# Performance work log

Hardware: AMD Instinct MI355X
Metric: run time of the kernel (lower is better)

Reference implementation:

```python
import jax, jax.numpy as jnp
import numpy as np

T, B, IDIM, CDIM, N, M = 512, 64, 256, 512, 128, 64
EPS = 1e-8


def setup_inputs() -> dict:
    key = jax.random.key(0)
    ks = jax.random.split(key, 16)
    stdev = 5.0 / np.sqrt(IDIM + M + CDIM)
    u = lambda k, s: jax.random.uniform(k, s, jnp.float32, -stdev, stdev)
    return {
        'embs': jax.random.normal(ks[0], (T, B, IDIM), jnp.float32),
        'W_ih': u(ks[1], (4 * CDIM, IDIM + M)),
        'W_hh': u(ks[2], (4 * CDIM, CDIM)),
        'b_ih': jnp.zeros((4 * CDIM,), jnp.float32),
        'b_hh': jnp.zeros((4 * CDIM,), jnp.float32),
        'W_kr': jax.random.normal(ks[3], (M, CDIM), jnp.float32) * 0.05,
        'b_kr': jnp.zeros((M,), jnp.float32),
        'w_br': jax.random.normal(ks[4], (CDIM,), jnp.float32) * 0.05,
        'W_kw': jax.random.normal(ks[5], (M, CDIM), jnp.float32) * 0.05,
        'b_kw': jnp.zeros((M,), jnp.float32),
        'w_bw': jax.random.normal(ks[6], (CDIM,), jnp.float32) * 0.05,
        'W_e': jax.random.normal(ks[7], (M, CDIM), jnp.float32) * 0.05,
        'b_e': jnp.zeros((M,), jnp.float32),
        'W_a': jax.random.normal(ks[8], (M, IDIM), jnp.float32) * 0.05,
        'b_a': jnp.zeros((M,), jnp.float32),
        'h0': jax.random.normal(ks[9], (CDIM,), jnp.float32) * 0.05,
        'c0': jax.random.normal(ks[10], (CDIM,), jnp.float32) * 0.05,
        'r0': jax.random.normal(ks[11], (M,), jnp.float32) * 0.02,
        'mem0': jax.random.normal(ks[12], (N, M), jnp.float32) * 0.01,
    }


def _address(Mem, k, beta):
    # Mem: [B,N,M], k: [B,M], beta: [B] -> content weights [B,N]
    sim = jnp.einsum('bnm,bm->bn', Mem, k)
    denom = jnp.linalg.norm(Mem, axis=2) * jnp.linalg.norm(k, axis=1)[:, None] + EPS
    return jax.nn.softmax(beta[:, None] * (sim / denom), axis=1)


def reference(embs, W_ih, W_hh, b_ih, b_hh, W_kr, b_kr, w_br, W_kw, b_kw,
              w_bw, W_e, b_e, W_a, b_a, h0, c0, r0, mem0):
    bsz = embs.shape[1]
    h = jnp.broadcast_to(h0, (bsz, CDIM))
    c = jnp.broadcast_to(c0, (bsz, CDIM))
    r = jnp.broadcast_to(r0, (bsz, M))
    Mem = jnp.broadcast_to(mem0, (bsz, N, M))

    def step(carry, emb):
        h, c, r, Mem = carry
        x = jnp.concatenate([emb, r], axis=1)            # [B, idim+M]
        gates = x @ W_ih.T + b_ih + h @ W_hh.T + b_hh    # [B, 4*cdim]
        i, f, g, o = jnp.split(gates, 4, axis=1)          # torch LSTM gate order
        i, f, o = jax.nn.sigmoid(i), jax.nn.sigmoid(f), jax.nn.sigmoid(o)
        g = jnp.tanh(g)
        c = f * c + i * g
        h = o * jnp.tanh(c)
        co = h                                            # controller output
        # write (erase/add, NTM content addressing)
        kw = jnp.tanh(co @ W_kw.T + b_kw)
        ww = _address(Mem, kw, jax.nn.softplus(co @ w_bw))
        e = jax.nn.sigmoid(co @ W_e.T + b_e)
        a = jnp.tanh(emb @ W_a.T + b_a)
        Mem = Mem * (1.0 - ww[:, :, None] * e[:, None, :]) + ww[:, :, None] * a[:, None, :]
        # read
        kr = jnp.tanh(co @ W_kr.T + b_kr)
        wr = _address(Mem, kr, jax.nn.softplus(co @ w_br))
        r = jnp.einsum('bn,bnm->bm', wr, Mem)
        out = jnp.concatenate([co, r], axis=1)            # [B, cdim+M]
        return (h, c, r, Mem), out

    _, os = jax.lax.scan(step, (h, c, r, Mem), embs)
    return os  # [T, B, cdim+M]
```

## Files before the change

kernel.cpp:

```cpp
#include <hip/hip_runtime.h>

#define TT 512
#define BB 64
#define IDIM 256
#define CDIM 512
#define NMEM 128
#define MDIM 64
#define KTOT 832
#define ODIM 576
#define NROWS 2048
#define NA 256
#define NB 64

struct Params {
  const float* embs; const float* W_ih; const float* W_hh; const float* b_ih; const float* b_hh;
  const float* W_kr; const float* b_kr; const float* w_br; const float* W_kw; const float* b_kw;
  const float* w_bw; const float* W_e; const float* b_e; const float* W_a; const float* b_a;
  const float* h0; const float* c0; const float* r0; const float* mem0;
  float* out;
  unsigned* flags;
  float* Wopt;
  float* h_buf;
  float* r_buf;
};

__device__ __forceinline__ float sigmoidf_(float x) { return 1.0f / (1.0f + __expf(-x)); }
__device__ __forceinline__ float tanhf_(float x) {
  float e = __expf(-2.0f * fabsf(x));
  float t = (1.0f - e) / (1.0f + e);
  return copysignf(t, x);
}
__device__ __forceinline__ float softplusf_(float x) {
  return (x > 20.0f) ? x : log1pf(__expf(x));
}
__device__ __forceinline__ float wred_sum(float v) {
#pragma unroll
  for (int off = 32; off > 0; off >>= 1) v += __shfl_xor(v, off, 64);
  return v;
}
__device__ __forceinline__ float wred_max(float v) {
#pragma unroll
  for (int off = 32; off > 0; off >>= 1) v = fmaxf(v, __shfl_xor(v, off, 64));
  return v;
}
__device__ __forceinline__ unsigned wred_minu(unsigned v) {
#pragma unroll
  for (int off = 32; off > 0; off >>= 1) {
    unsigned o = (unsigned)__shfl_xor((int)v, off, 64);
    v = (o < v) ? o : v;
  }
  return v;
}

__device__ __forceinline__ unsigned flag_ld(const unsigned* f) {
  return __hip_atomic_load(f, __ATOMIC_RELAXED, __HIP_MEMORY_SCOPE_AGENT);
}
__device__ __forceinline__ void st_wt(float* p, float v) {
  __hip_atomic_store(p, v, __ATOMIC_RELAXED, __HIP_MEMORY_SCOPE_AGENT);
}
__device__ __forceinline__ void flag_post(unsigned* f, unsigned val) {
  __hip_atomic_store(f, val, __ATOMIC_RELAXED, __HIP_MEMORY_SCOPE_AGENT);
}
__device__ __forceinline__ void drain_vm() {
  asm volatile("s_waitcnt vmcnt(0)" ::: "memory");
}
__device__ __forceinline__ float2 ld2_wt(const float* p) {
  unsigned long long v = __hip_atomic_load((const unsigned long long*)p,
                                           __ATOMIC_RELAXED, __HIP_MEMORY_SCOPE_AGENT);
  float2 r;
  r.x = __uint_as_float((unsigned)(v & 0xFFFFFFFFull));
  r.y = __uint_as_float((unsigned)(v >> 32));
  return r;
}

__device__ __forceinline__ void wait_group32(const unsigned* base, int lane, unsigned target) {
  for (;;) {
    unsigned v = (lane < 32) ? flag_ld(base + lane) : 0xFFFFFFFFu;
    v = wred_minu(v);
    if (v >= target) break;
    __builtin_amdgcn_s_sleep(1);
  }
  asm volatile("" ::: "memory");
}
__device__ __forceinline__ void wait_all256(const unsigned* f, int lane, unsigned target) {
  const unsigned* fp = f + lane * 4;
  for (;;) {
    unsigned a0 = flag_ld(fp + 0);
    unsigned a1 = flag_ld(fp + 1);
    unsigned a2 = flag_ld(fp + 2);
    unsigned a3 = flag_ld(fp + 3);
    unsigned m = a0 < a1 ? a0 : a1;
    unsigned n = a2 < a3 ? a2 : a3;
    m = m < n ? m : n;
    m = wred_minu(m);
    if (m >= target) break;
    __builtin_amdgcn_s_sleep(1);
  }
  asm volatile("" ::: "memory");
}
__device__ __forceinline__ void wait_all64(const unsigned* f, int lane, unsigned target) {
  const unsigned* fp = f + lane;
  for (;;) {
    unsigned b = flag_ld(fp);
    b = wred_minu(b);
    if (b >= target) break;
    __builtin_amdgcn_s_sleep(1);
  }
  asm volatile("" ::: "memory");
}

__global__ void __launch_bounds__(256) transpose_w_kernel(const float* __restrict__ W_ih,
                                                          const float* __restrict__ W_hh,
                                                          float* __restrict__ Wopt) {
  int idx = blockIdx.x * 256 + threadIdx.x;
  if (idx >= NROWS * KTOT) return;
  int lr = idx & 7;
  int rem = idx >> 3;
  int k = rem % KTOT;
  int w = rem / KTOT;
  int row = 512 * (lr >> 1) + 2 * w + (lr & 1);
  float v = (k < 320) ? W_ih[(size_t)row * 320 + k] : W_hh[(size_t)row * 512 + (k - 320)];
  Wopt[idx] = v;
}

struct AShared {
  float xs[64 * 65];
  float wsa[KTOT * 8];
  float bsum[8];
};
struct BShared {
  float Mem[MDIM][NMEM + 1];
  float hb[CDIM];
  float kw[MDIM], kr[MDIM], e[MDIM], a[MDIM];
  float ww[NMEM], wr[NMEM];
  float sc[8];
};
union SharedU { AShared a; BShared b; };

__global__ void __launch_bounds__(256) mann_kernel(Params p) {
  const int w = blockIdx.x;
  const int tid = threadIdx.x;
  const int lane = tid & 63;
  const int q = tid >> 6;

  unsigned* Aw = p.flags;
  unsigned* Bf = p.flags + 256;
  unsigned* Ar = p.flags + 320;

  __shared__ __align__(16) SharedU su;

  if (w < NA) {
    float* xs = su.a.xs;
    float* wsa = su.a.wsa;
    float* bsum = su.a.bsum;
    {
      const float4* src = (const float4*)(p.Wopt + (size_t)w * KTOT * 8);
      float4* dst = (float4*)wsa;
      for (int i = tid; i < KTOT * 2; i += 256) dst[i] = src[i];
    }
    if (tid < 8) {
      int row = 512 * (tid >> 1) + 2 * w + (tid & 1);
      bsum[tid] = p.b_ih[row] + p.b_hh[row];
    }
    float c_reg = 0.0f;
    if (tid < 128) {
      int jj = tid >> 6, b = tid & 63;
      int j = 2 * w + jj;
      c_reg = p.c0[j];
      st_wt(p.h_buf + (size_t)b * CDIM + j, p.h0[j]);
    }
    drain_vm();
    __syncthreads();
    if (tid == 0) {
      flag_post(&Aw[w], 1u);
      flag_post(&Ar[w], 1u);
    }

    const int kk4 = (tid & 15) * 4;
    const int bb0 = tid >> 4;

#pragma unroll 1
    for (int t = 0; t < TT; ++t) {
      float4 vbuf[4];
#pragma unroll
      for (int i = 0; i < 4; ++i) {
        const int b = bb0 + 16 * i;
        vbuf[i] = *(const float4*)(p.embs + ((size_t)t * BB + b) * IDIM + kk4);
      }

      const float* h_read = p.h_buf + (size_t)(t & 1) * (BB * CDIM);
      float* h_write = p.h_buf + (size_t)((t + 1) & 1) * (BB * CDIM);

      float acc[8];
#pragma unroll
      for (int i = 0; i < 8; ++i) acc[i] = 0.0f;

      int cur = 0;
#pragma unroll 1
      for (int ci = 0; ci < 12; ++ci) {
#pragma unroll
        for (int i = 0; i < 4; ++i) {
          const int b = bb0 + 16 * i;
          xs[(kk4 + 0) * 65 + b] = vbuf[i].x;
          xs[(kk4 + 1) * 65 + b] = vbuf[i].y;
          xs[(kk4 + 2) * 65 + b] = vbuf[i].z;
          xs[(kk4 + 3) * 65 + b] = vbuf[i].w;
        }
        __syncthreads();

        const int nxt = (cur == 3) ? 5 : cur + 1;
        if (ci < 11) {
          if (nxt >= 5) {
            wait_group32(Aw + (nxt - 5) * 32, lane, (unsigned)(t + 1));
            const int k = nxt * 64 + kk4 - 320;
#pragma unroll
            for (int i = 0; i < 4; ++i) {
              const int b = bb0 + 16 * i;
              const float* src = h_read + (size_t)b * CDIM + k;
              const float2 lo = ld2_wt(src);
              const float2 hi = ld2_wt(src + 2);
              vbuf[i].x = lo.x; vbuf[i].y = lo.y; vbuf[i].z = hi.x; vbuf[i].w = hi.y;
            }
          } else {
            const int k = nxt * 64 + kk4;
#pragma unroll
            for (int i = 0; i < 4; ++i) {
              const int b = bb0 + 16 * i;
              vbuf[i] = *(const float4*)(p.embs + ((size_t)t * BB + b) * IDIM + k);
            }
          }
        }

        const int kkb = 16 * q;
#pragma unroll
        for (int kki = 0; kki < 16; ++kki) {
          const int kk = kkb + kki;
          const float xv = xs[kk * 65 + lane];
          const float4 w0 = *(const float4*)&wsa[(cur * 64 + kk) * 8];
          const float4 w1 = *(const float4*)&wsa[(cur * 64 + kk) * 8 + 4];
          acc[0] = fmaf(xv, w0.x, acc[0]);
          acc[1] = fmaf(xv, w0.y, acc[1]);
          acc[2] = fmaf(xv, w0.z, acc[2]);
          acc[3] = fmaf(xv, w0.w, acc[3]);
          acc[4] = fmaf(xv, w1.x, acc[4]);
          acc[5] = fmaf(xv, w1.y, acc[5]);
          acc[6] = fmaf(xv, w1.z, acc[6]);
          acc[7] = fmaf(xv, w1.w, acc[7]);
        }
        __syncthreads();
        cur = nxt;
      }

      if (tid == 0) flag_post(&Ar[w], (unsigned)(t + 2));

      wait_all64(Bf, lane, (unsigned)(t + 1));
      {
#pragma unroll
        for (int i = 0; i < 4; ++i) {
          const int b = bb0 + 16 * i;
          const float* src = p.r_buf + b * MDIM + kk4;
          const float2 lo = ld2_wt(src);
          const float2 hi = ld2_wt(src + 2);
          vbuf[i].x = lo.x; vbuf[i].y = lo.y; vbuf[i].z = hi.x; vbuf[i].w = hi.y;
        }
#pragma unroll
        for (int i = 0; i < 4; ++i) {
          const int b = bb0 + 16 * i;
          xs[(kk4 + 0) * 65 + b] = vbuf[i].x;
          xs[(kk4 + 1) * 65 + b] = vbuf[i].y;
          xs[(kk4 + 2) * 65 + b] = vbuf[i].z;
          xs[(kk4 + 3) * 65 + b] = vbuf[i].w;
        }
        __syncthreads();
        const int kkb = 16 * q;
#pragma unroll
        for (int kki = 0; kki < 16; ++kki) {
          const int kk = kkb + kki;
          const float xv = xs[kk * 65 + lane];
          const float4 w0 = *(const float4*)&wsa[(4 * 64 + kk) * 8];
          const float4 w1 = *(const float4*)&wsa[(4 * 64 + kk) * 8 + 4];
          acc[0] = fmaf(xv, w0.x, acc[0]);
          acc[1] = fmaf(xv, w0.y, acc[1]);
          acc[2] = fmaf(xv, w0.z, acc[2]);
          acc[3] = fmaf(xv, w0.w, acc[3]);
          acc[4] = fmaf(xv, w1.x, acc[4]);
          acc[5] = fmaf(xv, w1.y, acc[5]);
          acc[6] = fmaf(xv, w1.z, acc[6]);
          acc[7] = fmaf(xv, w1.w, acc[7]);
        }
        __syncthreads();
      }

      {
        float* red = xs;
#pragma unroll
        for (int lr = 0; lr < 8; ++lr) red[(q * 8 + lr) * 64 + lane] = acc[lr];
        __syncthreads();
        if (tid < 64) wait_all256(Ar, lane, (unsigned)(t + 1));
        __syncthreads();
        if (tid < 128) {
          const int jj = tid >> 6, b = tid & 63;
          float g[4];
#pragma unroll
          for (int gate = 0; gate < 4; ++gate) {
            const int lr = gate * 2 + jj;
            float s = bsum[lr];
#pragma unroll
            for (int qq = 0; qq < 4; ++qq) s += red[(qq * 8 + lr) * 64 + b];
            g[gate] = s;
          }
          const float iv = sigmoidf_(g[0]);
          const float fv = sigmoidf_(g[1]);
          const float gv = tanhf_(g[2]);
          const float ov = sigmoidf_(g[3]);
          c_reg = fv * c_reg + iv * gv;
          const float hv = ov * tanhf_(c_reg);
          st_wt(h_write + (size_t)b * CDIM + 2 * w + jj, hv);
        }
      }
      drain_vm();
      __syncthreads();
      if (tid == 0) flag_post(&Aw[w], (unsigned)(t + 2));
    }
  } else {
    const int b = w - NA;
    float (&Mem_s)[MDIM][NMEM + 1] = su.b.Mem;
    float* hb = su.b.hb;
    float* kw_s = su.b.kw;
    float* kr_s = su.b.kr;
    float* e_s = su.b.e;
    float* a_s = su.b.a;
    float* ww_s = su.b.ww;
    float* wr_s = su.b.wr;
    float* sc = su.b.sc;

    for (int idx = tid; idx < NMEM * MDIM; idx += 256) {
      int n = idx >> 6, m = idx & 63;
      Mem_s[m][n] = p.mem0[idx];
    }
    if (tid < MDIM) st_wt(p.r_buf + b * MDIM + tid, p.r0[tid]);
    drain_vm();
    __syncthreads();
    if (tid == 0) flag_post(&Bf[b], 1u);

#pragma unroll 1
    for (int t = 0; t < TT; ++t) {
      float* h_src = p.h_buf + (size_t)((t + 1) & 1) * (BB * CDIM);

      if (q == 1) {
        const int m = lane;
        const float* Wrow = p.W_a + (size_t)m * IDIM;
        const float* eb = p.embs + ((size_t)t * BB + b) * IDIM;
        float s = p.b_a[m];
#pragma unroll 4
        for (int k = 0; k < IDIM; k += 4) {
          const float4 wv = *(const float4*)(Wrow + k);
          const float4 ev = *(const float4*)(eb + k);
          s = fmaf(wv.x, ev.x, s);
          s = fmaf(wv.y, ev.y, s);
          s = fmaf(wv.z, ev.z, s);
          s = fmaf(wv.w, ev.w, s);
        }
        a_s[m] = tanhf_(s);
      }
      if (tid < 64) wait_all256(Aw, lane, (unsigned)(t + 2));
      __syncthreads();

      {
        const float2 hv = ld2_wt(h_src + (size_t)b * CDIM + tid * 2);
        hb[tid * 2] = hv.x;
        hb[tid * 2 + 1] = hv.y;
      }
      __syncthreads();
      if (tid < 194) {
        const float* Wrow;
        if (tid < 64)        Wrow = p.W_kw + (size_t)tid * CDIM;
        else if (tid < 128)  Wrow = p.W_e + (size_t)(tid - 64) * CDIM;
        else if (tid < 192)  Wrow = p.W_kr + (size_t)(tid - 128) * CDIM;
        else if (tid == 192) Wrow = p.w_bw;
        else                 Wrow = p.w_br;
        float s = 0.0f;
#pragma unroll 4
        for (int k = 0; k < CDIM; k += 4) {
          const float4 wv = *(const float4*)(Wrow + k);
          s = fmaf(wv.x, hb[k], s);
          s = fmaf(wv.y, hb[k + 1], s);
          s = fmaf(wv.z, hb[k + 2], s);
          s = fmaf(wv.w, hb[k + 3], s);
        }
        if (tid < 64)       kw_s[tid] = tanhf_(s + p.b_kw[tid]);
        else if (tid < 128) e_s[tid - 64] = sigmoidf_(s + p.b_e[tid - 64]);
        else if (tid < 192) kr_s[tid - 128] = tanhf_(s + p.b_kr[tid - 128]);
        else                sc[tid - 192] = softplusf_(s);
      }
      __syncthreads();
      if (tid < 128) {
        const float v = (q == 0) ? kw_s[lane] : kr_s[lane];
        const float ss = wred_sum(v * v);
        if (lane == 0) sc[2 + q] = sqrtf(ss);
      }
      __syncthreads();
      {
        float logit = 0.0f, ex = 0.0f;
        const float beta = sc[0], keyn = sc[2];
        if (tid < 128) {
          float sim = 0.0f, nrm = 0.0f;
#pragma unroll 8
          for (int m = 0; m < MDIM; ++m) {
            const float mv = Mem_s[m][tid];
            sim = fmaf(mv, kw_s[m], sim);
            nrm = fmaf(mv, mv, nrm);
          }
          logit = beta * sim / (sqrtf(nrm) * keyn + 1e-8f);
          const float mx = wred_max(logit);
          if (lane == 0) sc[4 + q] = mx;
        }
        __syncthreads();
        if (tid < 128) {
          ex = __expf(logit - fmaxf(sc[4], sc[5]));
          const float sm = wred_sum(ex);
          if (lane == 0) sc[6 + q] = sm;
        }
        __syncthreads();
        if (tid < 128) ww_s[tid] = ex / (sc[6] + sc[7]);
        __syncthreads();
      }
      for (int idx = tid; idx < NMEM * MDIM; idx += 256) {
        const int m = idx >> 7, n = idx & 127;
        const float mv = Mem_s[m][n];
        Mem_s[m][n] = mv * (1.0f - ww_s[n] * e_s[m]) + ww_s[n] * a_s[m];
      }
      __syncthreads();
      {
        float logit = 0.0f, ex = 0.0f;
        const float beta = sc[1], keyn = sc[3];
        if (tid < 128) {
          float sim = 0.0f, nrm = 0.0f;
#pragma unroll 8
          for (int m = 0; m < MDIM; ++m) {
            const float mv = Mem_s[m][tid];
            sim = fmaf(mv, kr_s[m], sim);
            nrm = fmaf(mv, mv, nrm);
          }
          logit = beta * sim / (sqrtf(nrm) * keyn + 1e-8f);
          const float mx = wred_max(logit);
          if (lane == 0) sc[4 + q] = mx;
        }
        __syncthreads();
        if (tid < 128) {
          ex = __expf(logit - fmaxf(sc[4], sc[5]));
          const float sm = wred_sum(ex);
          if (lane == 0) sc[6 + q] = sm;
        }
        __syncthreads();
        if (tid < 128) wr_s[tid] = ex / (sc[6] + sc[7]);
        __syncthreads();
      }
      if (tid < 64) {
        float rv = 0.0f;
#pragma unroll 8
        for (int n = 0; n < NMEM; ++n) rv = fmaf(wr_s[n], Mem_s[tid][n], rv);
        st_wt(p.r_buf + b * MDIM + tid, rv);
        p.out[((size_t)t * BB + b) * ODIM + 512 + tid] = rv;
      }
      p.out[((size_t)t * BB + b) * ODIM + tid] = hb[tid];
      p.out[((size_t)t * BB + b) * ODIM + 256 + tid] = hb[tid + 256];
      drain_vm();
      __syncthreads();
      if (tid == 0) flag_post(&Bf[b], (unsigned)(t + 2));
    }
  }
}

extern "C" void kernel_launch(void* const* d_in, const int* in_sizes, int n_in,
                              void* d_out, int out_size, void* d_ws, size_t ws_size,
                              hipStream_t stream) {
  (void)in_sizes; (void)n_in; (void)out_size; (void)ws_size;
  Params p;
  p.embs = (const float*)d_in[0];
  p.W_ih = (const float*)d_in[1];
  p.W_hh = (const float*)d_in[2];
  p.b_ih = (const float*)d_in[3];
  p.b_hh = (const float*)d_in[4];
  p.W_kr = (const float*)d_in[5];
  p.b_kr = (const float*)d_in[6];
  p.w_br = (const float*)d_in[7];
  p.W_kw = (const float*)d_in[8];
  p.b_kw = (const float*)d_in[9];
  p.w_bw = (const float*)d_in[10];
  p.W_e  = (const float*)d_in[11];
  p.b_e  = (const float*)d_in[12];
  p.W_a  = (const float*)d_in[13];
  p.b_a  = (const float*)d_in[14];
  p.h0   = (const float*)d_in[15];
  p.c0   = (const float*)d_in[16];
  p.r0   = (const float*)d_in[17];
  p.mem0 = (const float*)d_in[18];
  p.out = (float*)d_out;

  float* ws = (float*)d_ws;
  p.flags = (unsigned*)ws;
  p.Wopt = ws + 1024;
  p.h_buf = p.Wopt + (size_t)NROWS * KTOT;
  p.r_buf = p.h_buf + 2 * BB * CDIM;

  hipMemsetAsync(p.flags, 0, 1024 * sizeof(unsigned), stream);

  const int total = NROWS * KTOT;
  hipLaunchKernelGGL(transpose_w_kernel, dim3((total + 255) / 256), dim3(256), 0, stream,
                     p.W_ih, p.W_hh, p.Wopt);

  void* kargs[] = { (void*)&p };
  hipError_t err = hipLaunchCooperativeKernel((const void*)mann_kernel, dim3(NA + NB), dim3(256),
                                              kargs, 0, stream);
  if (err != hipSuccess) {
    hipLaunchKernelGGL(mann_kernel, dim3(NA + NB), dim3(256), 0, stream, p);
  }
}
```

Baseline: 16.81 ms.

## Exchange hidden state as bf16 in triple buffer, drop read-ack barrier, deepen prefetch

Hidden state is now shared between blocks as packed bf16 in a three-slot ring buffer. This halves the cross-block traffic and lets the per-step Ar acknowledgement flags and their wait_all256 barrier be removed. The A-blocks' chunk loop now prefetches two chunks ahead with double-buffered registers. The B-blocks post their r-ready flag before writing outputs, so consumers can start earlier. Rounding h to bf16 adds a numerical error that compounds through the recurrence, and the three-slot ring buffer relies on the flag ordering being enough to prevent overwrite races.

```diff
diff --git a/kernel.cpp b/kernel.cpp
--- a/kernel.cpp
+++ b/kernel.cpp
@@ -11,6 +11,7 @@
 #define NROWS 2048
 #define NA 256
 #define NB 64
+#define H16S 256
 
 struct Params {
   const float* embs; const float* W_ih; const float* W_hh; const float* b_ih; const float* b_hh;
@@ -20,7 +21,7 @@
   float* out;
   unsigned* flags;
   float* Wopt;
-  float* h_buf;
+  unsigned* h16;
   float* r_buf;
 };
 
@@ -56,6 +57,9 @@
   return __hip_atomic_load(f, __ATOMIC_RELAXED, __HIP_MEMORY_SCOPE_AGENT);
 }
 __device__ __forceinline__ void st_wt(float* p, float v) {
+  __hip_atomic_store(p, v, __ATOMIC_RELAXED, __HIP_MEMORY_SCOPE_AGENT);
+}
+__device__ __forceinline__ void st_wt_u32(unsigned* p, unsigned v) {
   __hip_atomic_store(p, v, __ATOMIC_RELAXED, __HIP_MEMORY_SCOPE_AGENT);
 }
 __device__ __forceinline__ void flag_post(unsigned* f, unsigned val) {
@@ -71,6 +75,17 @@
   r.x = __uint_as_float((unsigned)(v & 0xFFFFFFFFull));
   r.y = __uint_as_float((unsigned)(v >> 32));
   return r;
+}
+__device__ __forceinline__ unsigned long long ld_u64_wt(const unsigned* p) {
+  return __hip_atomic_load((const unsigned long long*)p,
+                           __ATOMIC_RELAXED, __HIP_MEMORY_SCOPE_AGENT);
+}
+__device__ __forceinline__ unsigned ld_u32_wt(const unsigned* p) {
+  return __hip_atomic_load(p, __ATOMIC_RELAXED, __HIP_MEMORY_SCOPE_AGENT);
+}
+__device__ __forceinline__ unsigned f2bf(float x) {
+  unsigned u = __float_as_uint(x);
+  return (u + 0x7FFFu + ((u >> 16) & 1u)) >> 16;
 }
 
 __device__ __forceinline__ void wait_group32(const unsigned* base, int lane, unsigned target) {
@@ -145,7 +160,6 @@
 
   unsigned* Aw = p.flags;
   unsigned* Bf = p.flags + 256;
-  unsigned* Ar = p.flags + 320;
 
   __shared__ __align__(16) SharedU su;
 
@@ -162,82 +176,82 @@
       int row = 512 * (tid >> 1) + 2 * w + (tid & 1);
       bsum[tid] = p.b_ih[row] + p.b_hh[row];
     }
-    float c_reg = 0.0f;
-    if (tid < 128) {
-      int jj = tid >> 6, b = tid & 63;
-      int j = 2 * w + jj;
-      c_reg = p.c0[j];
-      st_wt(p.h_buf + (size_t)b * CDIM + j, p.h0[j]);
+    float2 c2 = make_float2(0.0f, 0.0f);
+    if (tid < 64) {
+      c2 = make_float2(p.c0[2 * w], p.c0[2 * w + 1]);
+      unsigned pk = f2bf(p.h0[2 * w]) | (f2bf(p.h0[2 * w + 1]) << 16);
+      st_wt_u32(p.h16 + (size_t)tid * H16S + w, pk);
     }
     drain_vm();
     __syncthreads();
-    if (tid == 0) {
-      flag_post(&Aw[w], 1u);
-      flag_post(&Ar[w], 1u);
-    }
+    if (tid == 0) flag_post(&Aw[w], 1u);
 
     const int kk4 = (tid & 15) * 4;
     const int bb0 = tid >> 4;
 
 #pragma unroll 1
     for (int t = 0; t < TT; ++t) {
-      float4 vbuf[4];
-#pragma unroll
-      for (int i = 0; i < 4; ++i) {
-        const int b = bb0 + 16 * i;
-        vbuf[i] = *(const float4*)(p.embs + ((size_t)t * BB + b) * IDIM + kk4);
-      }
-
-      const float* h_read = p.h_buf + (size_t)(t & 1) * (BB * CDIM);
-      float* h_write = p.h_buf + (size_t)((t + 1) & 1) * (BB * CDIM);
+      const unsigned* h16r = p.h16 + (size_t)(t % 3) * (BB * H16S);
+      unsigned* h16w = p.h16 + (size_t)((t + 1) % 3) * (BB * H16S);
+      const unsigned tgt = (unsigned)(t + 1);
+
+      float4 ev[2][4];
+      unsigned long long hv[2][4];
+
+      auto issue = [&](int cn, int s) {
+        if (cn < 4) {
+          const int k = cn * 64 + kk4;
+#pragma unroll
+          for (int i = 0; i < 4; ++i) {
+            const int b = bb0 + 16 * i;
+            ev[s][i] = *(const float4*)(p.embs + ((size_t)t * BB + b) * IDIM + k);
+          }
+        } else {
+          wait_group32(Aw + (cn - 5) * 32, lane, tgt);
+          const int slot = (cn * 32 - 160) + (tid & 15) * 2;
+#pragma unroll
+          for (int i = 0; i < 4; ++i) {
+            const int b = bb0 + 16 * i;
+            hv[s][i] = ld_u64_wt(h16r + (size_t)b * H16S + slot);
+          }
+        }
+      };
+      auto stage = [&](int cn, int s) {
+        if (cn < 4) {
+#pragma unroll
+          for (int i = 0; i < 4; ++i) {
+            const int b = bb0 + 16 * i;
+            xs[(kk4 + 0) * 65 + b] = ev[s][i].x;
+            xs[(kk4 + 1) * 65 + b] = ev[s][i].y;
+            xs[(kk4 + 2) * 65 + b] = ev[s][i].z;
+            xs[(kk4 + 3) * 65 + b] = ev[s][i].w;
+          }
+        } else {
+#pragma unroll
+          for (int i = 0; i < 4; ++i) {
+            const int b = bb0 + 16 * i;
+            const unsigned lo = (unsigned)hv[s][i];
+            const unsigned hi = (unsigned)(hv[s][i] >> 32);
+            xs[(kk4 + 0) * 65 + b] = __uint_as_float(lo << 16);
+            xs[(kk4 + 1) * 65 + b] = __uint_as_float(lo & 0xFFFF0000u);
+            xs[(kk4 + 2) * 65 + b] = __uint_as_float(hi << 16);
+            xs[(kk4 + 3) * 65 + b] = __uint_as_float(hi & 0xFFFF0000u);
+          }
+        }
+      };
 
       float acc[8];
 #pragma unroll
       for (int i = 0; i < 8; ++i) acc[i] = 0.0f;
 
-      int cur = 0;
-#pragma unroll 1
-      for (int ci = 0; ci < 12; ++ci) {
-#pragma unroll
-        for (int i = 0; i < 4; ++i) {
-          const int b = bb0 + 16 * i;
-          xs[(kk4 + 0) * 65 + b] = vbuf[i].x;
-          xs[(kk4 + 1) * 65 + b] = vbuf[i].y;
-          xs[(kk4 + 2) * 65 + b] = vbuf[i].z;
-          xs[(kk4 + 3) * 65 + b] = vbuf[i].w;
-        }
-        __syncthreads();
-
-        const int nxt = (cur == 3) ? 5 : cur + 1;
-        if (ci < 11) {
-          if (nxt >= 5) {
-            wait_group32(Aw + (nxt - 5) * 32, lane, (unsigned)(t + 1));
-            const int k = nxt * 64 + kk4 - 320;
-#pragma unroll
-            for (int i = 0; i < 4; ++i) {
-              const int b = bb0 + 16 * i;
-              const float* src = h_read + (size_t)b * CDIM + k;
-              const float2 lo = ld2_wt(src);
-              const float2 hi = ld2_wt(src + 2);
-              vbuf[i].x = lo.x; vbuf[i].y = lo.y; vbuf[i].z = hi.x; vbuf[i].w = hi.y;
-            }
-          } else {
-            const int k = nxt * 64 + kk4;
-#pragma unroll
-            for (int i = 0; i < 4; ++i) {
-              const int b = bb0 + 16 * i;
-              vbuf[i] = *(const float4*)(p.embs + ((size_t)t * BB + b) * IDIM + k);
-            }
-          }
-        }
-
+      auto compute = [&](int cn) {
         const int kkb = 16 * q;
 #pragma unroll
         for (int kki = 0; kki < 16; ++kki) {
           const int kk = kkb + kki;
           const float xv = xs[kk * 65 + lane];
-          const float4 w0 = *(const float4*)&wsa[(cur * 64 + kk) * 8];
-          const float4 w1 = *(const float4*)&wsa[(cur * 64 + kk) * 8 + 4];
+          const float4 w0 = *(const float4*)&wsa[(cn * 64 + kk) * 8];
+          const float4 w1 = *(const float4*)&wsa[(cn * 64 + kk) * 8 + 4];
           acc[0] = fmaf(xv, w0.x, acc[0]);
           acc[1] = fmaf(xv, w0.y, acc[1]);
           acc[2] = fmaf(xv, w0.z, acc[2]);
@@ -247,13 +261,25 @@
           acc[6] = fmaf(xv, w1.z, acc[6]);
           acc[7] = fmaf(xv, w1.w, acc[7]);
         }
-        __syncthreads();
-        cur = nxt;
-      }
-
-      if (tid == 0) flag_post(&Ar[w], (unsigned)(t + 2));
-
-      wait_all64(Bf, lane, (unsigned)(t + 1));
+      };
+
+      issue(0, 0);
+      issue(1, 1);
+#pragma unroll 1
+      for (int ci = 0; ci < 12; ++ci) {
+        const int cn = ci + (ci >= 4 ? 1 : 0);
+        stage(cn, ci & 1);
+        __syncthreads();
+        if (ci < 10) {
+          const int cn2 = (ci + 2) + (ci + 2 >= 4 ? 1 : 0);
+          issue(cn2, ci & 1);
+        }
+        compute(cn);
+        __syncthreads();
+      }
+
+      if (tid < 64) wait_all64(Bf, lane, tgt);
+      __syncthreads();
       {
 #pragma unroll
         for (int i = 0; i < 4; ++i) {
@@ -261,33 +287,13 @@
           const float* src = p.r_buf + b * MDIM + kk4;
           const float2 lo = ld2_wt(src);
           const float2 hi = ld2_wt(src + 2);
-          vbuf[i].x = lo.x; vbuf[i].y = lo.y; vbuf[i].z = hi.x; vbuf[i].w = hi.y;
-        }
-#pragma unroll
-        for (int i = 0; i < 4; ++i) {
-          const int b = bb0 + 16 * i;
-          xs[(kk4 + 0) * 65 + b] = vbuf[i].x;
-          xs[(kk4 + 1) * 65 + b] = vbuf[i].y;
-          xs[(kk4 + 2) * 65 + b] = vbuf[i].z;
-          xs[(kk4 + 3) * 65 + b] = vbuf[i].w;
-        }
-        __syncthreads();
-        const int kkb = 16 * q;
-#pragma unroll
-        for (int kki = 0; kki < 16; ++kki) {
-          const int kk = kkb + kki;
-          const float xv = xs[kk * 65 + lane];
-          const float4 w0 = *(const float4*)&wsa[(4 * 64 + kk) * 8];
-          const float4 w1 = *(const float4*)&wsa[(4 * 64 + kk) * 8 + 4];
-          acc[0] = fmaf(xv, w0.x, acc[0]);
-          acc[1] = fmaf(xv, w0.y, acc[1]);
-          acc[2] = fmaf(xv, w0.z, acc[2]);
-          acc[3] = fmaf(xv, w0.w, acc[3]);
-          acc[4] = fmaf(xv, w1.x, acc[4]);
-          acc[5] = fmaf(xv, w1.y, acc[5]);
-          acc[6] = fmaf(xv, w1.z, acc[6]);
-          acc[7] = fmaf(xv, w1.w, acc[7]);
-        }
+          xs[(kk4 + 0) * 65 + b] = lo.x;
+          xs[(kk4 + 1) * 65 + b] = lo.y;
+          xs[(kk4 + 2) * 65 + b] = hi.x;
+          xs[(kk4 + 3) * 65 + b] = hi.y;
+        }
+        __syncthreads();
+        compute(4);
         __syncthreads();
       }
 
@@ -296,26 +302,26 @@
 #pragma unroll
         for (int lr = 0; lr < 8; ++lr) red[(q * 8 + lr) * 64 + lane] = acc[lr];
         __syncthreads();
-        if (tid < 64) wait_all256(Ar, lane, (unsigned)(t + 1));
-        __syncthreads();
-        if (tid < 128) {
-          const int jj = tid >> 6, b = tid & 63;
-          float g[4];
-#pragma unroll
-          for (int gate = 0; gate < 4; ++gate) {
-            const int lr = gate * 2 + jj;
+        if (tid < 64) {
+          const int b = tid;
+          float g[8];
+#pragma unroll
+          for (int lr = 0; lr < 8; ++lr) {
             float s = bsum[lr];
 #pragma unroll
             for (int qq = 0; qq < 4; ++qq) s += red[(qq * 8 + lr) * 64 + b];
-            g[gate] = s;
-          }
-          const float iv = sigmoidf_(g[0]);
-          const float fv = sigmoidf_(g[1]);
-          const float gv = tanhf_(g[2]);
-          const float ov = sigmoidf_(g[3]);
-          c_reg = fv * c_reg + iv * gv;
-          const float hv = ov * tanhf_(c_reg);
-          st_wt(h_write + (size_t)b * CDIM + 2 * w + jj, hv);
+            g[lr] = s;
+          }
+          const float i0 = sigmoidf_(g[0]), f0 = sigmoidf_(g[2]);
+          const float g0 = tanhf_(g[4]), o0 = sigmoidf_(g[6]);
+          const float i1 = sigmoidf_(g[1]), f1 = sigmoidf_(g[3]);
+          const float g1 = tanhf_(g[5]), o1 = sigmoidf_(g[7]);
+          c2.x = f0 * c2.x + i0 * g0;
+          c2.y = f1 * c2.y + i1 * g1;
+          const float h0 = o0 * tanhf_(c2.x);
+          const float h1 = o1 * tanhf_(c2.y);
+          const unsigned pk = f2bf(h0) | (f2bf(h1) << 16);
+          st_wt_u32(h16w + (size_t)b * H16S + w, pk);
         }
       }
       drain_vm();
@@ -345,7 +351,7 @@
 
 #pragma unroll 1
     for (int t = 0; t < TT; ++t) {
-      float* h_src = p.h_buf + (size_t)((t + 1) & 1) * (BB * CDIM);
+      const unsigned* hsrc = p.h16 + (size_t)((t + 1) % 3) * (BB * H16S) + (size_t)b * H16S;
 
       if (q == 1) {
         const int m = lane;
@@ -355,11 +361,11 @@
 #pragma unroll 4
         for (int k = 0; k < IDIM; k += 4) {
           const float4 wv = *(const float4*)(Wrow + k);
-          const float4 ev = *(const float4*)(eb + k);
-          s = fmaf(wv.x, ev.x, s);
-          s = fmaf(wv.y, ev.y, s);
-          s = fmaf(wv.z, ev.z, s);
-          s = fmaf(wv.w, ev.w, s);
+          const float4 evv = *(const float4*)(eb + k);
+          s = fmaf(wv.x, evv.x, s);
+          s = fmaf(wv.y, evv.y, s);
+          s = fmaf(wv.z, evv.z, s);
+          s = fmaf(wv.w, evv.w, s);
         }
         a_s[m] = tanhf_(s);
       }
@@ -367,9 +373,9 @@
       __syncthreads();
 
       {
-        const float2 hv = ld2_wt(h_src + (size_t)b * CDIM + tid * 2);
-        hb[tid * 2] = hv.x;
-        hb[tid * 2 + 1] = hv.y;
+        const unsigned v = ld_u32_wt(hsrc + tid);
+        hb[2 * tid] = __uint_as_float(v << 16);
+        hb[2 * tid + 1] = __uint_as_float(v & 0xFFFF0000u);
       }
       __syncthreads();
       if (tid < 194) {
@@ -456,18 +462,18 @@
         if (tid < 128) wr_s[tid] = ex / (sc[6] + sc[7]);
         __syncthreads();
       }
+      float rv = 0.0f;
       if (tid < 64) {
-        float rv = 0.0f;
 #pragma unroll 8
         for (int n = 0; n < NMEM; ++n) rv = fmaf(wr_s[n], Mem_s[tid][n], rv);
         st_wt(p.r_buf + b * MDIM + tid, rv);
-        p.out[((size_t)t * BB + b) * ODIM + 512 + tid] = rv;
-      }
+      }
+      drain_vm();
+      __syncthreads();
+      if (tid == 0) flag_post(&Bf[b], (unsigned)(t + 2));
+      if (tid < 64) p.out[((size_t)t * BB + b) * ODIM + 512 + tid] = rv;
       p.out[((size_t)t * BB + b) * ODIM + tid] = hb[tid];
       p.out[((size_t)t * BB + b) * ODIM + 256 + tid] = hb[tid + 256];
-      drain_vm();
-      __syncthreads();
-      if (tid == 0) flag_post(&Bf[b], (unsigned)(t + 2));
     }
   }
 }
@@ -501,8 +507,8 @@
   float* ws = (float*)d_ws;
   p.flags = (unsigned*)ws;
   p.Wopt = ws + 1024;
-  p.h_buf = p.Wopt + (size_t)NROWS * KTOT;
-  p.r_buf = p.h_buf + 2 * BB * CDIM;
+  p.h16 = (unsigned*)(p.Wopt + (size_t)NROWS * KTOT);
+  p.r_buf = (float*)(p.h16 + 3 * BB * H16S);
 
   hipMemsetAsync(p.flags, 0, 1024 * sizeof(unsigned), stream);
 
```

Result: faster. 15.25 ms (-9.3%).
